# Kernel tuning notes

Measured on AMD Instinct MI355X. Metric: run time of the kernel, lower is better.

The kernel has to match this reference:

```python
import jax, jax.numpy as jnp
import numpy as np

H = 1152  # hidden_size
NH = 16   # num_attention_heads
HD = H // NH  # head_dim = 72
FF = 4304  # intermediate_size
EPS = 1e-6
S = 4096
B = 1
NDOCS = 32


def _linear_params(key, d_in, d_out):
    kw, kb = jax.random.split(key)
    lim = 1.0 / np.sqrt(d_in)
    w = jax.random.uniform(kw, (d_out, d_in), jnp.float32, -lim, lim)
    b = jax.random.uniform(kb, (d_out,), jnp.float32, -lim, lim)
    return w, b


def setup_inputs() -> dict:
    key = jax.random.key(0)
    ks = jax.random.split(key, 8)
    hidden_states = jax.random.normal(ks[0], (B, S, H), jnp.float32)
    document_ids = jnp.sort(jax.random.randint(ks[1], (S,), 0, NDOCS))
    q_w, q_b = _linear_params(ks[2], H, H)
    k_w, k_b = _linear_params(ks[3], H, H)
    v_w, v_b = _linear_params(ks[4], H, H)
    o_w, o_b = _linear_params(ks[5], H, H)
    fc1_w, fc1_b = _linear_params(ks[6], H, FF)
    fc2_w, fc2_b = _linear_params(ks[7], FF, H)
    return {
        'hidden_states': hidden_states,
        'document_ids': document_ids,
        'q_w': q_w, 'q_b': q_b, 'k_w': k_w, 'k_b': k_b,
        'v_w': v_w, 'v_b': v_b, 'o_w': o_w, 'o_b': o_b,
        'ln1_g': jnp.ones((H,), jnp.float32), 'ln1_b': jnp.zeros((H,), jnp.float32),
        'ln2_g': jnp.ones((H,), jnp.float32), 'ln2_b': jnp.zeros((H,), jnp.float32),
        'fc1_w': fc1_w, 'fc1_b': fc1_b, 'fc2_w': fc2_w, 'fc2_b': fc2_b,
    }


def _layer_norm(x, g, b):
    mu = jnp.mean(x, axis=-1, keepdims=True)
    var = jnp.mean(jnp.square(x - mu), axis=-1, keepdims=True)
    return (x - mu) * jax.lax.rsqrt(var + EPS) * g + b


def _forward(hidden_states, q_w, q_b, k_w, k_b, v_w, v_b, o_w, o_b,
             ln1_g, ln1_b, ln2_g, ln2_b, fc1_w, fc1_b, fc2_w, fc2_b,
             document_ids):
    b, s, _ = hidden_states.shape
    scale = HD ** -0.5

    residual = hidden_states
    x = _layer_norm(hidden_states, ln1_g, ln1_b)

    # projections (torch Linear: y = x @ W.T + b)
    q = (x @ q_w.T + q_b).reshape(b, s, NH, HD).transpose(0, 2, 1, 3)
    k = (x @ k_w.T + k_b).reshape(b, s, NH, HD).transpose(0, 2, 1, 3)
    v = (x @ v_w.T + v_b).reshape(b, s, NH, HD).transpose(0, 2, 1, 3)

    # document-masked attention: attend only within same document id
    scores = jnp.einsum('bhqd,bhkd->bhqk', q, k) * scale
    mask = document_ids[:, None] == document_ids[None, :]  # [s, s]
    scores = jnp.where(mask[None, None], scores, -jnp.inf)
    attn = jax.nn.softmax(scores, axis=-1)
    out = jnp.einsum('bhqk,bhkd->bhqd', attn, v)  # [b,h,s,d]
    out = out.transpose(0, 2, 1, 3).reshape(b, s, H)
    out = out @ o_w.T + o_b

    hidden = residual + out
    residual = hidden
    x = _layer_norm(hidden, ln2_g, ln2_b)
    x = jax.nn.gelu(x @ fc1_w.T + fc1_b, approximate=True)
    x = x @ fc2_w.T + fc2_b
    return residual + x


def reference(hidden_states, document_ids, q_w, q_b, k_w, k_b, v_w, v_b,
              o_w, o_b, ln1_g, ln1_b, ln2_g, ln2_b, fc1_w, fc1_b, fc2_w, fc2_b):
    return _forward(hidden_states, q_w, q_b, k_w, k_b, v_w, v_b, o_w, o_b,
                    ln1_g, ln1_b, ln2_g, ln2_b, fc1_w, fc1_b, fc2_w, fc2_b,
                    document_ids)
```

## Files before the change

kernel.cpp:

```cpp
#include <hip/hip_runtime.h>

typedef unsigned short u16;
typedef unsigned int u32;
typedef __attribute__((ext_vector_type(8))) __bf16 bf16x8;
typedef __attribute__((ext_vector_type(8))) u16 u16x8;
typedef __attribute__((ext_vector_type(4))) float f32x4;
typedef __attribute__((ext_vector_type(2))) u32 u32x2;

#define SEQ 4096
#define HID 1152
#define NHEAD 16
#define HDIM 72
#define FF 4304
#define FFP 4352
#define H3 3456

__device__ __forceinline__ u16 f2bf(float f) {
  u32 u = __builtin_bit_cast(u32, f);
  u32 r = u + 0x7fffu + ((u >> 16) & 1u);
  return (u16)(r >> 16);
}
__device__ __forceinline__ float bf2f(u16 h) {
  return __builtin_bit_cast(float, (u32)h << 16);
}
__device__ __forceinline__ float bflo(u32 u) { return __builtin_bit_cast(float, u << 16); }
__device__ __forceinline__ float bfhi(u32 u) { return __builtin_bit_cast(float, u & 0xffff0000u); }

typedef const __attribute__((address_space(1))) void* gas_t;
typedef __attribute__((address_space(3))) void* las_t;
__device__ __forceinline__ void load_lds16(const void* g, void* l) {
  __builtin_amdgcn_global_load_lds((gas_t)(unsigned long long)g,
                                   (las_t)(u32)(unsigned long long)l, 16, 0, 0);
}

__device__ __forceinline__ float gelu_tanh(float x) {
  float t = tanhf(0.7978845608f * (x + 0.044715f * x * x * x));
  return 0.5f * x * (1.f + t);
}

__global__ __launch_bounds__(256) void cvt4_k(const float* __restrict__ in,
                                              u16* __restrict__ out, int n4) {
  int i = blockIdx.x * 256 + threadIdx.x;
  if (i >= n4) return;
  f32x4 f = ((const f32x4*)in)[i];
  u32x2 o;
  o[0] = (u32)f2bf(f[0]) | ((u32)f2bf(f[1]) << 16);
  o[1] = (u32)f2bf(f[2]) | ((u32)f2bf(f[3]) << 16);
  ((u32x2*)out)[i] = o;
}

__global__ __launch_bounds__(256) void cvt4_pad_k(const float* __restrict__ in,
                                                  u16* __restrict__ out,
                                                  int rows, int sc, int dc) {
  int i = blockIdx.x * 256 + threadIdx.x;
  long long n4 = (long long)rows * dc / 4;
  if (i >= n4) return;
  long long idx = (long long)i * 4;
  int r = (int)(idx / dc);
  int c = (int)(idx % dc);
  u32x2 o;
  if (c < sc) {
    f32x4 f = *(const f32x4*)(in + (size_t)r * sc + c);
    o[0] = (u32)f2bf(f[0]) | ((u32)f2bf(f[1]) << 16);
    o[1] = (u32)f2bf(f[2]) | ((u32)f2bf(f[3]) << 16);
  } else {
    o[0] = 0; o[1] = 0;
  }
  ((u32x2*)out)[i] = o;
}

__global__ __launch_bounds__(256) void pack_bias_k(const float* __restrict__ qb,
                                                   const float* __restrict__ kb,
                                                   const float* __restrict__ vb,
                                                   const float* __restrict__ f1b,
                                                   float* __restrict__ bqkv,
                                                   float* __restrict__ bf1,
                                                   float* __restrict__ zbuf) {
  int i = blockIdx.x * 256 + threadIdx.x;
  if (i < H3) bqkv[i] = (i < HID) ? qb[i] : (i < 2 * HID ? kb[i - HID] : vb[i - 2 * HID]);
  if (i < FFP) bf1[i] = (i < FF) ? f1b[i] : 0.f;
  if (i < 16) zbuf[i] = 0.f;
}

__global__ __launch_bounds__(256) void docrange_k(const int* __restrict__ ids,
                                                  int* __restrict__ se) {
  int i = blockIdx.x * 256 + threadIdx.x;
  if (i >= SEQ) return;
  int id = ids[i];
  int lo = 0, hi = SEQ;
  while (lo < hi) { int mid = (lo + hi) >> 1; if (ids[mid] < id) lo = mid + 1; else hi = mid; }
  int s = lo;
  lo = 0; hi = SEQ;
  while (lo < hi) { int mid = (lo + hi) >> 1; if (ids[mid] <= id) lo = mid + 1; else hi = mid; }
  se[2 * i] = s;
  se[2 * i + 1] = lo;
}

__global__ __launch_bounds__(256) void ln_k(const float* __restrict__ x,
                                            const float* __restrict__ g,
                                            const float* __restrict__ b,
                                            u16* __restrict__ y) {
  __shared__ float sred[8];
  int row = blockIdx.x, tid = threadIdx.x;
  const f32x4* xr = (const f32x4*)(x + (size_t)row * HID);
  f32x4 v0 = {}, v1 = {};
  float s = 0.f, s2 = 0.f;
  int c0 = tid, c1 = tid + 256;
  v0 = xr[c0];
  if (c1 < 288) v1 = xr[c1];
#pragma unroll
  for (int j = 0; j < 4; ++j) { s += v0[j] + v1[j]; s2 += v0[j] * v0[j] + v1[j] * v1[j]; }
#pragma unroll
  for (int sh = 32; sh; sh >>= 1) { s += __shfl_xor(s, sh); s2 += __shfl_xor(s2, sh); }
  if ((tid & 63) == 0) { sred[tid >> 6] = s; sred[4 + (tid >> 6)] = s2; }
  __syncthreads();
  s = sred[0] + sred[1] + sred[2] + sred[3];
  s2 = sred[4] + sred[5] + sred[6] + sred[7];
  float mu = s * (1.f / HID);
  float rs = rsqrtf(s2 * (1.f / HID) - mu * mu + 1e-6f);
  u16* yr = y + (size_t)row * HID;
  const f32x4* g4 = (const f32x4*)g;
  const f32x4* b4 = (const f32x4*)b;
  {
    f32x4 gv = g4[c0], bv = b4[c0];
    u32x2 o;
    o[0] = (u32)f2bf((v0[0] - mu) * rs * gv[0] + bv[0]) |
           ((u32)f2bf((v0[1] - mu) * rs * gv[1] + bv[1]) << 16);
    o[1] = (u32)f2bf((v0[2] - mu) * rs * gv[2] + bv[2]) |
           ((u32)f2bf((v0[3] - mu) * rs * gv[3] + bv[3]) << 16);
    *(u32x2*)(yr + c0 * 4) = o;
  }
  if (c1 < 288) {
    f32x4 gv = g4[c1], bv = b4[c1];
    u32x2 o;
    o[0] = (u32)f2bf((v1[0] - mu) * rs * gv[0] + bv[0]) |
           ((u32)f2bf((v1[1] - mu) * rs * gv[1] + bv[1]) << 16);
    o[1] = (u32)f2bf((v1[2] - mu) * rs * gv[2] + bv[2]) |
           ((u32)f2bf((v1[3] - mu) * rs * gv[3] + bv[3]) << 16);
    *(u32x2*)(yr + c1 * 4) = o;
  }
}

template <int EP>
__global__ __launch_bounds__(256, 2) void gemm_bt(const u16* __restrict__ A,
                                                  const u16* __restrict__ B,
                                                  void* __restrict__ outp,
                                                  const float* __restrict__ bias,
                                                  const float* __restrict__ resid,
                                                  int M, int N, int K) {
  __shared__ u16 As[128 * 32];
  __shared__ u16 Bs[128 * 32];
  int tid = threadIdx.x;
  int l = tid & 63, w = tid >> 6;
  int nxy = gridDim.x * gridDim.y;
  int bidf = blockIdx.y * gridDim.x + blockIdx.x;
  int cpx = nxy >> 3;
  bidf = (bidf & 7) * cpx + (bidf >> 3);
  int m0 = (bidf / gridDim.x) * 128;
  int n0 = (bidf % gridDim.x) * 128;
  int wr = w >> 1, wc = w & 1;
  f32x4 acc[4][4] = {};
  int offr = tid >> 2;
  int offc = (tid & 3) * 16;
  const char* Ab0 = (const char*)A + ((size_t)(m0 + offr) * K) * 2 + offc;
  const char* Ab1 = (const char*)A + ((size_t)(m0 + 64 + offr) * K) * 2 + offc;
  const char* Bb0 = (const char*)B + ((size_t)(n0 + offr) * K) * 2 + offc;
  const char* Bb1 = (const char*)B + ((size_t)(n0 + 64 + offr) * K) * 2 + offc;
  char* AsW = (char*)As + w * 1024;
  char* BsW = (char*)Bs + w * 1024;
  const char* Ar = (const char*)As + (wr * 64 + (l & 15)) * 64 + (l >> 4) * 16;
  const char* Br = (const char*)Bs + (wc * 64 + (l & 15)) * 64 + (l >> 4) * 16;
  int k0 = 0, kend = K;
  if (EP == 5) {
    int nz = gridDim.z;
    int ksp = ((K / 32 + nz - 1) / nz) * 32;
    k0 = blockIdx.z * ksp;
    kend = min(K, k0 + ksp);
  }
  for (int kt = k0; kt < kend; kt += 32) {
    size_t kb = (size_t)kt * 2;
    load_lds16(Ab0 + kb, AsW);
    load_lds16(Ab1 + kb, AsW + 4096);
    load_lds16(Bb0 + kb, BsW);
    load_lds16(Bb1 + kb, BsW + 4096);
    __syncthreads();
    bf16x8 af[4], bfr[4];
#pragma unroll
    for (int m = 0; m < 4; ++m) af[m] = *(const bf16x8*)(Ar + m * 16 * 64);
#pragma unroll
    for (int n = 0; n < 4; ++n) bfr[n] = *(const bf16x8*)(Br + n * 16 * 64);
#pragma unroll
    for (int m = 0; m < 4; ++m)
#pragma unroll
      for (int n = 0; n < 4; ++n)
        acc[m][n] = __builtin_amdgcn_mfma_f32_16x16x32_bf16(af[m], bfr[n], acc[m][n], 0, 0, 0);
    __syncthreads();
  }
#pragma unroll
  for (int m = 0; m < 4; ++m) {
    int row = m0 + wr * 64 + m * 16 + (l >> 4) * 4;
#pragma unroll
    for (int n = 0; n < 4; ++n) {
      int col = n0 + wc * 64 + n * 16 + (l & 15);
      float bv = (EP == 5) ? 0.f : bias[col];
      if (EP == 4) {
        int region = (col >= 2304) ? 2 : (col >= 1152 ? 1 : 0);
        int cw = col - region * 1152;
        int hh = cw / 72;
        int dd = cw - hh * 72;
        u16* dst = (u16*)outp + (((size_t)region * NHEAD + hh) * SEQ) * HDIM + dd;
#pragma unroll
        for (int j = 0; j < 4; ++j)
          dst[(size_t)(row + j) * HDIM] = f2bf(acc[m][n][j] + bv);
      } else if (EP == 5) {
        u16* P = (u16*)outp + (size_t)blockIdx.z * M * N;
#pragma unroll
        for (int j = 0; j < 4; ++j)
          P[(size_t)(row + j) * N + col] = f2bf(acc[m][n][j]);
      } else {
#pragma unroll
        for (int j = 0; j < 4; ++j) {
          size_t idx = (size_t)(row + j) * N + col;
          float v = acc[m][n][j] + bv;
          if (EP == 1) ((u16*)outp)[idx] = f2bf(gelu_tanh(v));
          else ((float*)outp)[idx] = v + resid[idx];
        }
      }
    }
  }
}

template <int NS>
__global__ __launch_bounds__(256) void splitk_reduce_k(const u16* __restrict__ P,
                                                       const float* __restrict__ bias,
                                                       const float* __restrict__ resid,
                                                       float* __restrict__ out, int n4) {
  int i = blockIdx.x * 256 + threadIdx.x;
  if (i >= n4) return;
  size_t base = (size_t)i * 4;
  int col = (int)(base % HID);
  f32x4 a = {};
#pragma unroll
  for (int s = 0; s < NS; ++s) {
    u32x2 pv = *(const u32x2*)(P + (size_t)s * SEQ * HID + base);
    a[0] += bflo(pv[0]);
    a[1] += bfhi(pv[0]);
    a[2] += bflo(pv[1]);
    a[3] += bfhi(pv[1]);
  }
  f32x4 bv = *(const f32x4*)(bias + col);
  f32x4 rv = ((const f32x4*)resid)[i];
  ((f32x4*)out)[i] = a + bv + rv;
}

__device__ __forceinline__ u32 swz(u32 a) { return a ^ (((a >> 8) & 7u) << 4); }

__global__ __launch_bounds__(256, 2) void attn_mfma_k(const u16* __restrict__ qkvh,
                                                      const int* __restrict__ se,
                                                      const float* __restrict__ zb,
                                                      u16* __restrict__ outb) {
  __shared__ u16 Ks[128 * 104];
  __shared__ u16 Vt[80 * 128];
  __shared__ u16 Ps[4][16 * 128];
  __shared__ int Sq[64], Eq[64];
  int tid = threadIdx.x, l = tid & 63, w = tid >> 6;
  int h = blockIdx.y, q0 = blockIdx.x * 64;
  const float scale = 0.1178511302f;
  const u16* Qh = qkvh + (size_t)h * SEQ * HDIM;
  const u16* Kh = qkvh + ((size_t)NHEAD + h) * SEQ * HDIM;
  const u16* Vh = qkvh + ((size_t)2 * NHEAD + h) * SEQ * HDIM;

  for (int i = tid; i < 512; i += 256) ((u32*)(Vt + 72 * 128))[i] = 0;

#pragma unroll
  for (int it = 0; it < 4; ++it) {
    int cw0 = it * 256 + w * 64;
    if (cw0 < 832) {
      int chunk = cw0 + l;
      int row = chunk / 13, c16 = chunk - row * 13;
      const void* src = (c16 < 9)
                            ? (const void*)(Qh + ((size_t)(q0 + row)) * HDIM + c16 * 8)
                            : (const void*)zb;
      load_lds16(src, (char*)Ks + (size_t)cw0 * 16);
    }
  }
  if (tid < 64) { Sq[tid] = se[2 * (q0 + tid)]; Eq[tid] = se[2 * (q0 + tid) + 1]; }
  __syncthreads();

  int sqj[4], eqj[4];
#pragma unroll
  for (int j = 0; j < 4; ++j) {
    int ql = w * 16 + (l >> 4) * 4 + j;
    sqj[j] = Sq[ql]; eqj[j] = Eq[ql];
  }
  const char* Aq = (const char*)Ks + (w * 16 + (l & 15)) * 208 + (l >> 4) * 16;
  bf16x8 aq[3];
#pragma unroll
  for (int dsl = 0; dsl < 3; ++dsl) aq[dsl] = *(const bf16x8*)(Aq + dsl * 64);
  __syncthreads();

  int kmin = se[2 * q0];
  int kmax = se[2 * (q0 + 63) + 1];
  f32x4 o[5] = {};
  float m_run[4], l_run[4];
#pragma unroll
  for (int j = 0; j < 4; ++j) { m_run[j] = -1e30f; l_run[j] = 0.f; }

  for (int kc = kmin; kc < kmax; kc += 128) {
#pragma unroll
    for (int it = 0; it < 7; ++it) {
      int cw0 = it * 256 + w * 64;
      if (cw0 < 1664) {
        int chunk = cw0 + l;
        int row = chunk / 13, c16 = chunk - row * 13;
        int krow = kc + row;
        const void* src = (c16 < 9 && krow < SEQ)
                              ? (const void*)(Kh + (size_t)krow * HDIM + c16 * 8)
                              : (const void*)zb;
        load_lds16(src, (char*)Ks + (size_t)cw0 * 16);
      }
    }
#pragma unroll
    for (int it = 0; it < 3; ++it) {
      int idx = it * 256 + tid;
      if (idx < 576) {
        int k2 = idx / 9, d8 = idx - k2 * 9;
        int kr0 = kc + 2 * k2, kr1 = kr0 + 1;
        kr0 = kr0 < SEQ ? kr0 : SEQ - 1;
        kr1 = kr1 < SEQ ? kr1 : SEQ - 1;
        u16x8 r0 = *(const u16x8*)(Vh + (size_t)kr0 * HDIM + d8 * 8);
        u16x8 r1 = *(const u16x8*)(Vh + (size_t)kr1 * HDIM + d8 * 8);
#pragma unroll
        for (int j = 0; j < 8; ++j) {
          u32 pr = (u32)r0[j] | ((u32)r1[j] << 16);
          *(u32*)((char*)Vt + swz((u32)(d8 * 8 + j) * 256 + (u32)k2 * 4)) = pr;
        }
      }
    }
    __syncthreads();

    f32x4 sf[8];
#pragma unroll
    for (int kt = 0; kt < 8; ++kt) {
      const char* Bk = (const char*)Ks + (kt * 16 + (l & 15)) * 208 + (l >> 4) * 16;
      f32x4 acc = {};
      acc = __builtin_amdgcn_mfma_f32_16x16x32_bf16(aq[0], *(const bf16x8*)Bk, acc, 0, 0, 0);
      acc = __builtin_amdgcn_mfma_f32_16x16x32_bf16(aq[1], *(const bf16x8*)(Bk + 64), acc, 0, 0, 0);
      acc = __builtin_amdgcn_mfma_f32_16x16x32_bf16(aq[2], *(const bf16x8*)(Bk + 128), acc, 0, 0, 0);
      sf[kt] = acc;
    }
    float mx[4] = {-1e30f, -1e30f, -1e30f, -1e30f};
#pragma unroll
    for (int kt = 0; kt < 8; ++kt) {
      int key = kc + kt * 16 + (l & 15);
#pragma unroll
      for (int j = 0; j < 4; ++j) {
        float s = sf[kt][j] * scale;
        bool valid = (key >= sqj[j]) && (key < eqj[j]);
        s = valid ? s : -1e30f;
        sf[kt][j] = s;
        mx[j] = fmaxf(mx[j], s);
      }
    }
#pragma unroll
    for (int j = 0; j < 4; ++j) {
      float m = mx[j];
      m = fmaxf(m, __shfl_xor(m, 1));
      m = fmaxf(m, __shfl_xor(m, 2));
      m = fmaxf(m, __shfl_xor(m, 4));
      m = fmaxf(m, __shfl_xor(m, 8));
      mx[j] = m;
    }
    float fz[4], ps[4];
#pragma unroll
    for (int j = 0; j < 4; ++j) {
      float mn = fmaxf(m_run[j], mx[j]);
      fz[j] = __expf(m_run[j] - mn);
      m_run[j] = mn;
      ps[j] = 0.f;
    }
#pragma unroll
    for (int kt = 0; kt < 8; ++kt)
#pragma unroll
      for (int j = 0; j < 4; ++j) {
        float s = sf[kt][j];
        float p = (s > -1e29f) ? __expf(s - m_run[j]) : 0.f;
        sf[kt][j] = p;
        ps[j] += p;
      }
#pragma unroll
    for (int j = 0; j < 4; ++j) {
      float p = ps[j];
      p += __shfl_xor(p, 1);
      p += __shfl_xor(p, 2);
      p += __shfl_xor(p, 4);
      p += __shfl_xor(p, 8);
      l_run[j] = l_run[j] * fz[j] + p;
#pragma unroll
      for (int dt = 0; dt < 5; ++dt) o[dt][j] *= fz[j];
    }
    char* PB = (char*)Ps[w];
#pragma unroll
    for (int kt = 0; kt < 8; ++kt)
#pragma unroll
      for (int j = 0; j < 4; ++j) {
        u32 a = (u32)((l >> 4) * 4 + j) * 256 + (u32)(kt * 16 + (l & 15)) * 2;
        *(u16*)(PB + swz(a)) = f2bf(sf[kt][j]);
      }
#pragma unroll
    for (int ks = 0; ks < 4; ++ks) {
      u32 aa = (u32)(l & 15) * 256 + (u32)((l >> 4) * 8 + ks * 32) * 2;
      bf16x8 ap = *(const bf16x8*)(PB + swz(aa));
#pragma unroll
      for (int dt = 0; dt < 5; ++dt) {
        u32 ba = (u32)(dt * 16 + (l & 15)) * 256 + (u32)((l >> 4) * 8 + ks * 32) * 2;
        bf16x8 bv = *(const bf16x8*)((const char*)Vt + swz(ba));
        o[dt] = __builtin_amdgcn_mfma_f32_16x16x32_bf16(ap, bv, o[dt], 0, 0, 0);
      }
    }
    __syncthreads();
  }

  float inv[4];
#pragma unroll
  for (int j = 0; j < 4; ++j) inv[j] = 1.f / l_run[j];
#pragma unroll
  for (int dt = 0; dt < 5; ++dt) {
    int d = dt * 16 + (l & 15);
    if (d < HDIM) {
#pragma unroll
      for (int j = 0; j < 4; ++j) {
        int q = q0 + w * 16 + (l >> 4) * 4 + j;
        outb[(size_t)q * HID + h * HDIM + d] = f2bf(o[dt][j] * inv[j]);
      }
    }
  }
}

constexpr size_t SZ_WQKV = (size_t)H3 * HID * 2;
constexpr size_t SZ_WO   = (size_t)HID * HID * 2;
constexpr size_t SZ_WF1  = (size_t)FFP * HID * 2;
constexpr size_t SZ_WF2  = (size_t)HID * FFP * 2;
constexpr size_t OFF_WQKV = 0;
constexpr size_t OFF_WO   = OFF_WQKV + SZ_WQKV;
constexpr size_t OFF_WF1  = OFF_WO + SZ_WO;
constexpr size_t OFF_BQKV = OFF_WF1 + SZ_WF1;
constexpr size_t OFF_BF1  = OFF_BQKV + (size_t)H3 * 4;
constexpr size_t OFF_SE   = OFF_BF1 + (size_t)FFP * 4;
constexpr size_t OFF_ZB   = OFF_SE + (size_t)SEQ * 2 * 4;
constexpr size_t OFF_XLN  = OFF_ZB + 64;
constexpr size_t OFF_QKV  = OFF_XLN + (size_t)SEQ * HID * 2;
constexpr size_t OFF_ACT  = OFF_QKV;
constexpr size_t OFF_AOUT = OFF_QKV + (size_t)SEQ * H3 * 2;
constexpr size_t OFF_HD   = OFF_AOUT + (size_t)SEQ * HID * 2;
constexpr size_t OFF_WF2  = OFF_HD + (size_t)SEQ * HID * 4;
constexpr size_t WS_NEED  = OFF_WF2 + SZ_WF2;
constexpr size_t OFF_P    = 0;
static_assert(OFF_ACT + (size_t)SEQ * FFP * 2 <= OFF_HD, "ACT must not clobber HD");
static_assert(3 * (size_t)SEQ * HID * 2 <= OFF_QKV, "P must stay in dead prefix");

extern "C" void kernel_launch(void* const* d_in, const int* in_sizes, int n_in,
                              void* d_out, int out_size, void* d_ws, size_t ws_size,
                              hipStream_t stream) {
  const float* hs   = (const float*)d_in[0];
  const int*   ids  = (const int*)d_in[1];
  const float* q_w  = (const float*)d_in[2];
  const float* q_b  = (const float*)d_in[3];
  const float* k_w  = (const float*)d_in[4];
  const float* k_b  = (const float*)d_in[5];
  const float* v_w  = (const float*)d_in[6];
  const float* v_b  = (const float*)d_in[7];
  const float* o_w  = (const float*)d_in[8];
  const float* o_b  = (const float*)d_in[9];
  const float* ln1g = (const float*)d_in[10];
  const float* ln1b = (const float*)d_in[11];
  const float* ln2g = (const float*)d_in[12];
  const float* ln2b = (const float*)d_in[13];
  const float* f1w  = (const float*)d_in[14];
  const float* f1b  = (const float*)d_in[15];
  const float* f2w  = (const float*)d_in[16];
  const float* f2b  = (const float*)d_in[17];

  if (ws_size < WS_NEED) return;

  char* ws = (char*)d_ws;
  u16*   Wqkv = (u16*)(ws + OFF_WQKV);
  u16*   Wo   = (u16*)(ws + OFF_WO);
  u16*   Wf1  = (u16*)(ws + OFF_WF1);
  u16*   Wf2  = (u16*)(ws + OFF_WF2);
  float* Bqkv = (float*)(ws + OFF_BQKV);
  float* Bf1  = (float*)(ws + OFF_BF1);
  int*   SE   = (int*)(ws + OFF_SE);
  float* ZB   = (float*)(ws + OFF_ZB);
  u16*   XLN  = (u16*)(ws + OFF_XLN);
  u16*   QKVh = (u16*)(ws + OFF_QKV);
  u16*   ACT  = (u16*)(ws + OFF_ACT);
  u16*   AOUT = (u16*)(ws + OFF_AOUT);
  float* HD   = (float*)(ws + OFF_HD);
  u16*   Pp   = (u16*)(ws + OFF_P);

  docrange_k<<<dim3(SEQ / 256), dim3(256), 0, stream>>>(ids, SE);

  int nW = HID * HID;
  cvt4_k<<<dim3((nW / 4 + 255) / 256), dim3(256), 0, stream>>>(q_w, Wqkv, nW / 4);
  cvt4_k<<<dim3((nW / 4 + 255) / 256), dim3(256), 0, stream>>>(k_w, Wqkv + nW, nW / 4);
  cvt4_k<<<dim3((nW / 4 + 255) / 256), dim3(256), 0, stream>>>(v_w, Wqkv + 2 * nW, nW / 4);
  cvt4_k<<<dim3((nW / 4 + 255) / 256), dim3(256), 0, stream>>>(o_w, Wo, nW / 4);
  {
    int n4 = FFP * HID / 4;
    cvt4_pad_k<<<dim3((n4 + 255) / 256), dim3(256), 0, stream>>>(f1w, Wf1, 1, FF * HID, FFP * HID);
  }
  {
    int n4 = HID * FFP / 4;
    cvt4_pad_k<<<dim3((n4 + 255) / 256), dim3(256), 0, stream>>>(f2w, Wf2, HID, FF, FFP);
  }
  pack_bias_k<<<dim3((FFP + 255) / 256), dim3(256), 0, stream>>>(q_b, k_b, v_b, f1b, Bqkv, Bf1, ZB);

  ln_k<<<dim3(SEQ), dim3(256), 0, stream>>>(hs, ln1g, ln1b, XLN);
  gemm_bt<4><<<dim3(H3 / 128, SEQ / 128), dim3(256), 0, stream>>>(XLN, Wqkv, QKVh, Bqkv, nullptr,
                                                                  SEQ, H3, HID);
  attn_mfma_k<<<dim3(SEQ / 64, NHEAD), dim3(256), 0, stream>>>(QKVh, SE, ZB, AOUT);
  gemm_bt<2><<<dim3(HID / 128, SEQ / 128), dim3(256), 0, stream>>>(AOUT, Wo, HD, o_b, hs,
                                                                   SEQ, HID, HID);
  ln_k<<<dim3(SEQ), dim3(256), 0, stream>>>(HD, ln2g, ln2b, XLN);
  gemm_bt<1><<<dim3(FFP / 128, SEQ / 128), dim3(256), 0, stream>>>(XLN, Wf1, ACT, Bf1, nullptr,
                                                                   SEQ, FFP, HID);
  gemm_bt<5><<<dim3(HID / 128, SEQ / 128, 3), dim3(256), 0, stream>>>(ACT, Wf2, Pp, nullptr,
                                                                      nullptr, SEQ, HID, FFP);
  splitk_reduce_k<3><<<dim3(SEQ * HID / 4 / 256), dim3(256), 0, stream>>>(Pp, f2b, HD,
                                                                          (float*)d_out,
                                                                          SEQ * HID / 4);
}
```

Measured before the change: 312.5 us.

## Double GEMM K-tile with XOR-swizzled LDS, fuse prep kernels, faster GELU

The bf16 GEMM now stages a 64-wide K slice per iteration instead of 32. Its LDS layout uses an XOR swizzle on 16-byte chunks to avoid bank conflicts, which halves the number of barrier pairs per K loop at the cost of twice the shared memory per block. Separately, the four square-weight conversions are merged into one 2D-grid launch, and doc-range search is merged with bias packing to cut launch overhead. The tanh-based GELU is replaced by an equivalent x*sigmoid(2z) form using __expf. The merged conversion assumes Wo sits contiguously after Wqkv in the workspace.

```diff
diff --git a/kernel.cpp b/kernel.cpp
--- a/kernel.cpp
+++ b/kernel.cpp
@@ -33,20 +33,24 @@
                                    (las_t)(u32)(unsigned long long)l, 16, 0, 0);
 }
 
-__device__ __forceinline__ float gelu_tanh(float x) {
-  float t = tanhf(0.7978845608f * (x + 0.044715f * x * x * x));
-  return 0.5f * x * (1.f + t);
-}
-
-__global__ __launch_bounds__(256) void cvt4_k(const float* __restrict__ in,
-                                              u16* __restrict__ out, int n4) {
+__device__ __forceinline__ float gelu_fast(float x) {
+  float z = 0.7978845608f * (x + 0.044715f * x * x * x);
+  return x / (1.f + __expf(-2.f * z));
+}
+
+__global__ __launch_bounds__(256) void cvt4x4_k(const float* __restrict__ a,
+                                                const float* __restrict__ b,
+                                                const float* __restrict__ c,
+                                                const float* __restrict__ d,
+                                                u16* __restrict__ out, int n4) {
   int i = blockIdx.x * 256 + threadIdx.x;
   if (i >= n4) return;
+  const float* in = (blockIdx.y == 0) ? a : (blockIdx.y == 1) ? b : (blockIdx.y == 2) ? c : d;
   f32x4 f = ((const f32x4*)in)[i];
   u32x2 o;
   o[0] = (u32)f2bf(f[0]) | ((u32)f2bf(f[1]) << 16);
   o[1] = (u32)f2bf(f[2]) | ((u32)f2bf(f[3]) << 16);
-  ((u32x2*)out)[i] = o;
+  ((u32x2*)(out + (size_t)blockIdx.y * n4 * 4))[i] = o;
 }
 
 __global__ __launch_bounds__(256) void cvt4_pad_k(const float* __restrict__ in,
@@ -69,31 +73,29 @@
   ((u32x2*)out)[i] = o;
 }
 
-__global__ __launch_bounds__(256) void pack_bias_k(const float* __restrict__ qb,
-                                                   const float* __restrict__ kb,
-                                                   const float* __restrict__ vb,
-                                                   const float* __restrict__ f1b,
-                                                   float* __restrict__ bqkv,
-                                                   float* __restrict__ bf1,
-                                                   float* __restrict__ zbuf) {
+__global__ __launch_bounds__(256) void prep_k(const int* __restrict__ ids,
+                                              const float* __restrict__ qb,
+                                              const float* __restrict__ kb,
+                                              const float* __restrict__ vb,
+                                              const float* __restrict__ f1b,
+                                              int* __restrict__ se,
+                                              float* __restrict__ bqkv,
+                                              float* __restrict__ bf1,
+                                              float* __restrict__ zbuf) {
   int i = blockIdx.x * 256 + threadIdx.x;
   if (i < H3) bqkv[i] = (i < HID) ? qb[i] : (i < 2 * HID ? kb[i - HID] : vb[i - 2 * HID]);
   if (i < FFP) bf1[i] = (i < FF) ? f1b[i] : 0.f;
   if (i < 16) zbuf[i] = 0.f;
-}
-
-__global__ __launch_bounds__(256) void docrange_k(const int* __restrict__ ids,
-                                                  int* __restrict__ se) {
-  int i = blockIdx.x * 256 + threadIdx.x;
-  if (i >= SEQ) return;
-  int id = ids[i];
-  int lo = 0, hi = SEQ;
-  while (lo < hi) { int mid = (lo + hi) >> 1; if (ids[mid] < id) lo = mid + 1; else hi = mid; }
-  int s = lo;
-  lo = 0; hi = SEQ;
-  while (lo < hi) { int mid = (lo + hi) >> 1; if (ids[mid] <= id) lo = mid + 1; else hi = mid; }
-  se[2 * i] = s;
-  se[2 * i + 1] = lo;
+  if (i < SEQ) {
+    int id = ids[i];
+    int lo = 0, hi = SEQ;
+    while (lo < hi) { int mid = (lo + hi) >> 1; if (ids[mid] < id) lo = mid + 1; else hi = mid; }
+    int s = lo;
+    lo = 0; hi = SEQ;
+    while (lo < hi) { int mid = (lo + hi) >> 1; if (ids[mid] <= id) lo = mid + 1; else hi = mid; }
+    se[2 * i] = s;
+    se[2 * i + 1] = lo;
+  }
 }
 
 __global__ __launch_bounds__(256) void ln_k(const float* __restrict__ x,
@@ -148,8 +150,8 @@
                                                   const float* __restrict__ bias,
                                                   const float* __restrict__ resid,
                                                   int M, int N, int K) {
-  __shared__ u16 As[128 * 32];
-  __shared__ u16 Bs[128 * 32];
+  __shared__ u16 As[128 * 64];
+  __shared__ u16 Bs[128 * 64];
   int tid = threadIdx.x;
   int l = tid & 63, w = tid >> 6;
   int nxy = gridDim.x * gridDim.y;
@@ -160,40 +162,45 @@
   int n0 = (bidf % gridDim.x) * 128;
   int wr = w >> 1, wc = w & 1;
   f32x4 acc[4][4] = {};
-  int offr = tid >> 2;
-  int offc = (tid & 3) * 16;
-  const char* Ab0 = (const char*)A + ((size_t)(m0 + offr) * K) * 2 + offc;
-  const char* Ab1 = (const char*)A + ((size_t)(m0 + 64 + offr) * K) * 2 + offc;
-  const char* Bb0 = (const char*)B + ((size_t)(n0 + offr) * K) * 2 + offc;
-  const char* Bb1 = (const char*)B + ((size_t)(n0 + 64 + offr) * K) * 2 + offc;
-  char* AsW = (char*)As + w * 1024;
-  char* BsW = (char*)Bs + w * 1024;
-  const char* Ar = (const char*)As + (wr * 64 + (l & 15)) * 64 + (l >> 4) * 16;
-  const char* Br = (const char*)Bs + (wc * 64 + (l & 15)) * 64 + (l >> 4) * 16;
+  int srow = tid >> 3;
+  int scol = ((tid & 7) * 16) ^ ((srow & 7) << 4);
+  const char* Ab = (const char*)A + ((size_t)(m0 + srow) * K) * 2 + scol;
+  const char* Bb = (const char*)B + ((size_t)(n0 + srow) * K) * 2 + scol;
+  char* AsD = (char*)As + w * 1024;
+  char* BsD = (char*)Bs + w * 1024;
+  const char* ArB = (const char*)As + (wr * 64 + (l & 15)) * 128;
+  const char* BrB = (const char*)Bs + (wc * 64 + (l & 15)) * 128;
+  int c0 = ((l >> 4) * 16) ^ ((l & 7) << 4);
+  int c1 = c0 ^ 64;
   int k0 = 0, kend = K;
   if (EP == 5) {
     int nz = gridDim.z;
-    int ksp = ((K / 32 + nz - 1) / nz) * 32;
+    int ksp = ((K / 64 + nz - 1) / nz) * 64;
     k0 = blockIdx.z * ksp;
     kend = min(K, k0 + ksp);
   }
-  for (int kt = k0; kt < kend; kt += 32) {
+  for (int kt = k0; kt < kend; kt += 64) {
     size_t kb = (size_t)kt * 2;
-    load_lds16(Ab0 + kb, AsW);
-    load_lds16(Ab1 + kb, AsW + 4096);
-    load_lds16(Bb0 + kb, BsW);
-    load_lds16(Bb1 + kb, BsW + 4096);
+#pragma unroll
+    for (int i = 0; i < 4; ++i) {
+      load_lds16(Ab + (size_t)i * 32 * K * 2 + kb, AsD + i * 4096);
+      load_lds16(Bb + (size_t)i * 32 * K * 2 + kb, BsD + i * 4096);
+    }
     __syncthreads();
-    bf16x8 af[4], bfr[4];
-#pragma unroll
-    for (int m = 0; m < 4; ++m) af[m] = *(const bf16x8*)(Ar + m * 16 * 64);
-#pragma unroll
-    for (int n = 0; n < 4; ++n) bfr[n] = *(const bf16x8*)(Br + n * 16 * 64);
-#pragma unroll
-    for (int m = 0; m < 4; ++m)
-#pragma unroll
-      for (int n = 0; n < 4; ++n)
-        acc[m][n] = __builtin_amdgcn_mfma_f32_16x16x32_bf16(af[m], bfr[n], acc[m][n], 0, 0, 0);
+#pragma unroll
+    for (int kk = 0; kk < 2; ++kk) {
+      int ck = kk ? c1 : c0;
+      bf16x8 af[4], bfr[4];
+#pragma unroll
+      for (int m = 0; m < 4; ++m) af[m] = *(const bf16x8*)(ArB + m * 2048 + ck);
+#pragma unroll
+      for (int n = 0; n < 4; ++n) bfr[n] = *(const bf16x8*)(BrB + n * 2048 + ck);
+#pragma unroll
+      for (int m = 0; m < 4; ++m)
+#pragma unroll
+        for (int n = 0; n < 4; ++n)
+          acc[m][n] = __builtin_amdgcn_mfma_f32_16x16x32_bf16(af[m], bfr[n], acc[m][n], 0, 0, 0);
+    }
     __syncthreads();
   }
 #pragma unroll
@@ -222,7 +229,7 @@
         for (int j = 0; j < 4; ++j) {
           size_t idx = (size_t)(row + j) * N + col;
           float v = acc[m][n][j] + bv;
-          if (EP == 1) ((u16*)outp)[idx] = f2bf(gelu_tanh(v));
+          if (EP == 1) ((u16*)outp)[idx] = f2bf(gelu_fast(v));
           else ((float*)outp)[idx] = v + resid[idx];
         }
       }
@@ -485,7 +492,6 @@
 
   char* ws = (char*)d_ws;
   u16*   Wqkv = (u16*)(ws + OFF_WQKV);
-  u16*   Wo   = (u16*)(ws + OFF_WO);
   u16*   Wf1  = (u16*)(ws + OFF_WF1);
   u16*   Wf2  = (u16*)(ws + OFF_WF2);
   float* Bqkv = (float*)(ws + OFF_BQKV);
@@ -498,14 +504,12 @@
   u16*   AOUT = (u16*)(ws + OFF_AOUT);
   float* HD   = (float*)(ws + OFF_HD);
   u16*   Pp   = (u16*)(ws + OFF_P);
-
-  docrange_k<<<dim3(SEQ / 256), dim3(256), 0, stream>>>(ids, SE);
-
+  u16*   Wo   = (u16*)(ws + OFF_WO);
+
+  prep_k<<<dim3((FFP + 255) / 256), dim3(256), 0, stream>>>(ids, q_b, k_b, v_b, f1b, SE, Bqkv,
+                                                            Bf1, ZB);
   int nW = HID * HID;
-  cvt4_k<<<dim3((nW / 4 + 255) / 256), dim3(256), 0, stream>>>(q_w, Wqkv, nW / 4);
-  cvt4_k<<<dim3((nW / 4 + 255) / 256), dim3(256), 0, stream>>>(k_w, Wqkv + nW, nW / 4);
-  cvt4_k<<<dim3((nW / 4 + 255) / 256), dim3(256), 0, stream>>>(v_w, Wqkv + 2 * nW, nW / 4);
-  cvt4_k<<<dim3((nW / 4 + 255) / 256), dim3(256), 0, stream>>>(o_w, Wo, nW / 4);
+  cvt4x4_k<<<dim3(nW / 4 / 256, 4), dim3(256), 0, stream>>>(q_w, k_w, v_w, o_w, Wqkv, nW / 4);
   {
     int n4 = FFP * HID / 4;
     cvt4_pad_k<<<dim3((n4 + 255) / 256), dim3(256), 0, stream>>>(f1w, Wf1, 1, FF * HID, FFP * HID);
@@ -514,7 +518,6 @@
     int n4 = HID * FFP / 4;
     cvt4_pad_k<<<dim3((n4 + 255) / 256), dim3(256), 0, stream>>>(f2w, Wf2, HID, FF, FFP);
   }
-  pack_bias_k<<<dim3((FFP + 255) / 256), dim3(256), 0, stream>>>(q_b, k_b, v_b, f1b, Bqkv, Bf1, ZB);
 
   ln_k<<<dim3(SEQ), dim3(256), 0, stream>>>(hs, ln1g, ln1b, XLN);
   gemm_bt<4><<<dim3(H3 / 128, SEQ / 128), dim3(256), 0, stream>>>(XLN, Wqkv, QKVh, Bqkv, nullptr,
```

New measurement: 293.0 us. 6.2% less time.
